# Kernel tuning notes

Measured on AMD Instinct MI355X. Metric: run time of the kernel, lower is better.

Reference implementation:

```python
import jax, jax.numpy as jnp
import numpy as np

N = 100000
IN_DIM, HID_DIM, EMB_DIM = 128, 64, 32
E = 1600000


def _gcn_conv(x, W, b, src, tgt, n):
    """PyG GCNConv: linear transform, add self-loops, sym-normalized scatter-add.
    W: [in, out], b: [out]. src/tgt: [E'] incl. self-loops handled by caller."""
    h = x @ W  # [n, out] -- transform before propagate (PyG order)
    deg = jax.ops.segment_sum(jnp.ones_like(tgt, dtype=h.dtype), tgt, num_segments=n)
    dinv = jnp.where(deg > 0, jax.lax.rsqrt(deg), 0.0)
    norm = dinv[src] * dinv[tgt]  # [E']
    msgs = h[src] * norm[:, None]  # [E', out]
    out = jax.ops.segment_sum(msgs, tgt, num_segments=n)
    return out + b


def setup_inputs() -> dict:
    key = jax.random.key(0)
    ks = jax.random.split(key, 6)
    x = jax.random.normal(ks[0], (N, IN_DIM), dtype=jnp.float32)
    edge_index = jax.random.randint(ks[1], (2, E), 0, N, dtype=jnp.int64)
    s1 = 1.0 / np.sqrt(IN_DIM)
    s2 = 1.0 / np.sqrt(HID_DIM)
    W1 = jax.random.uniform(ks[2], (IN_DIM, HID_DIM), jnp.float32, -s1, s1)
    b1 = jnp.zeros((HID_DIM,), jnp.float32)
    W2 = jax.random.uniform(ks[3], (HID_DIM, EMB_DIM), jnp.float32, -s2, s2)
    b2 = jnp.zeros((EMB_DIM,), jnp.float32)
    return {"x": x, "W1": W1, "b1": b1, "W2": W2, "b2": b2, "edge_index": edge_index}


def reference(x, W1, b1, W2, b2, edge_index):
    n = x.shape[0]
    src, tgt = edge_index[0], edge_index[1]
    # add self-loops once (same graph used by both convs)
    loops = jnp.arange(n, dtype=edge_index.dtype)
    src_sl = jnp.concatenate([src, loops])
    tgt_sl = jnp.concatenate([tgt, loops])
    h = jax.nn.relu(_gcn_conv(x, W1, b1, src_sl, tgt_sl, n))
    z = _gcn_conv(h, W2, b2, src_sl, tgt_sl, n)  # [n, EMB_DIM]
    # decode on original edges: edge-wise dot product
    recon = jnp.sum(z[src] * z[tgt], axis=1)  # [E]
    return z, recon
```

## Files before the change

kernel.cpp:

```cpp
#include <hip/hip_runtime.h>
#include <hip/hip_fp16.h>
#include <math.h>


#define NBMAX 512
#define BSHIFT 8
#define BNODES 256
#define CH 4096
#define CAPSHIFT 13
#define CAP (1 << CAPSHIFT)

typedef _Float16 half8 __attribute__((ext_vector_type(8)));
typedef float floatx4 __attribute__((ext_vector_type(4)));

static inline int divup(int a, int b) { return (a + b - 1) / b; }

__device__ inline void acc8(__half2* a, float4 v) {
    const __half2* h = (const __half2*)&v;
    a[0] = __hadd2(a[0], h[0]);
    a[1] = __hadd2(a[1], h[1]);
    a[2] = __hadd2(a[2], h[2]);
    a[3] = __hadd2(a[3], h[3]);
}
__device__ inline unsigned short f2bf(float f) {
    unsigned u = __builtin_bit_cast(unsigned, f);
    u = (u + 0x7FFFu + ((u >> 16) & 1u)) >> 16;
    return (unsigned short)u;
}


__global__ void k_init(int* __restrict__ gcur, unsigned* __restrict__ hs_pad,
                       unsigned* __restrict__ zs_pad) {
    int t = threadIdx.x;
    for (int b = t; b < NBMAX; b += 256) gcur[b] = b << CAPSHIFT;
    if (t < 32) hs_pad[t] = 0;
    else if (t < 48) zs_pad[t - 32] = 0;
}


__global__ __launch_bounds__(256) void k_part(const int* __restrict__ src,
                                              const int* __restrict__ tgt,
                                              int* __restrict__ gcur,
                                              unsigned* __restrict__ ebuf, int E, int NB) {
    __shared__ int h[NBMAX];
    __shared__ int base[NBMAX];
    int tid = threadIdx.x;
    int e0 = blockIdx.x * CH;
    for (int b = tid; b < NB; b += 256) h[b] = 0;
    __syncthreads();
    unsigned pk[16];
    int sv[16];
#pragma unroll
    for (int r = 0; r < 4; r++) {
        int e = e0 + (r * 256 + tid) * 4;
        if (e + 3 < E) {
            int4 t4 = *(const int4*)(tgt + e);
            int4 s4 = *(const int4*)(src + e);
            int tv[4] = {t4.x, t4.y, t4.z, t4.w};
            int sw[4] = {s4.x, s4.y, s4.z, s4.w};
#pragma unroll
            for (int j = 0; j < 4; j++) {
                int t = tv[j];
                int b = t >> BSHIFT;
                int l = atomicAdd(&h[b], 1);
                pk[r * 4 + j] = ((unsigned)b << 21) |
                                ((unsigned)(t & (BNODES - 1)) << 12) | (unsigned)l;
                sv[r * 4 + j] = sw[j];
            }
        } else {
#pragma unroll
            for (int j = 0; j < 4; j++) {
                int ee = e + j;
                if (ee < E) {
                    int t = tgt[ee];
                    int b = t >> BSHIFT;
                    int l = atomicAdd(&h[b], 1);
                    pk[r * 4 + j] = ((unsigned)b << 21) |
                                    ((unsigned)(t & (BNODES - 1)) << 12) | (unsigned)l;
                    sv[r * 4 + j] = src[ee];
                } else {
                    pk[r * 4 + j] = 0xFFFFFFFFu;
                }
            }
        }
    }
    __syncthreads();
    for (int b = tid; b < NB; b += 256) {
        int c = h[b];
        base[b] = c ? atomicAdd(&gcur[b], c) : 0;
    }
    __syncthreads();
#pragma unroll
    for (int i = 0; i < 16; i++) {
        if (pk[i] != 0xFFFFFFFFu) {
            int b = pk[i] >> 21;
            unsigned lt = (pk[i] >> 12) & (BNODES - 1);
            int l = pk[i] & 4095;
            ebuf[base[b] + l] = (lt << 23) | (unsigned)sv[i];
        }
    }
}


__global__ __launch_bounds__(256) void k_bfill(const unsigned* __restrict__ ebuf,
                                               const int* __restrict__ gcur,
                                               int* __restrict__ rowbeg,
                                               int* __restrict__ rowend,
                                               int* __restrict__ col,
                                               float* __restrict__ dinv, int n) {
    __shared__ int s_cnt[BNODES];
    __shared__ int s_scan[BNODES];
    __shared__ int s_cur[BNODES];
    int b = blockIdx.x, tid = threadIdx.x;
    int nbase = b << BSHIFT;
    int ebase = b << CAPSHIFT;
    int eend = gcur[b];
    s_cnt[tid] = 0;
    __syncthreads();
    for (int e = ebase + tid; e < eend; e += BNODES) {
        atomicAdd(&s_cnt[ebuf[e] >> 23], 1);
    }
    __syncthreads();
    s_scan[tid] = s_cnt[tid];
    __syncthreads();
    for (int off = 1; off < BNODES; off <<= 1) {
        int t = (tid >= off) ? s_scan[tid - off] : 0;
        __syncthreads();
        s_scan[tid] += t;
        __syncthreads();
    }
    int excl = s_scan[tid] - s_cnt[tid];
    s_cur[tid] = excl;
    int node = nbase + tid;
    if (node < n) {
        rowbeg[node] = ebase + excl;
        rowend[node] = ebase + excl + s_cnt[tid];
        dinv[node] = rsqrtf((float)(s_cnt[tid] + 1));
    }
    __syncthreads();
    for (int e = ebase + tid; e < eend; e += BNODES) {
        unsigned p = ebuf[e];
        int pos = atomicAdd(&s_cur[p >> 23], 1);
        col[ebase + pos] = (int)(p & 0x7FFFFFu);
    }
}


__global__ __launch_bounds__(256) void k_mm1(const float* __restrict__ x,
                                             const float* __restrict__ W1,
                                             const float* __restrict__ dinv,
                                             __half* __restrict__ hs, int n) {
    __shared__ _Float16 xh[64 * 136];
    __shared__ _Float16 Wt[64 * 136];
    int tid = threadIdx.x;
    int nbase = blockIdx.x * 64;
#pragma unroll
    for (int i = 0; i < 8; i++) {
        int f = tid + i * 256;
        int r = f >> 5, c4 = f & 31;
        int node = nbase + r;
        float4 v = make_float4(0.f, 0.f, 0.f, 0.f);
        if (node < n) v = *(const float4*)(x + (size_t)node * 128 + c4 * 4);
        union { uint2 u; __half2 h[2]; } pk;
        pk.h[0] = __floats2half2_rn(v.x, v.y);
        pk.h[1] = __floats2half2_rn(v.z, v.w);
        *(uint2*)&xh[r * 136 + c4 * 4] = pk.u;
    }
#pragma unroll
    for (int i = 0; i < 16; i++) {
        int f = tid + i * 256;
        int c = f & 63, kp = f >> 6;
        float a = W1[(size_t)(2 * kp) * 64 + c];
        float b = W1[(size_t)(2 * kp + 1) * 64 + c];
        *(__half2*)&Wt[c * 136 + 2 * kp] = __floats2half2_rn(a, b);
    }
    __syncthreads();
    int w = tid >> 6, lane = tid & 63;
    int quad = lane >> 4, m = lane & 15;
    floatx4 acc[4] = {{0.f, 0.f, 0.f, 0.f}, {0.f, 0.f, 0.f, 0.f},
                      {0.f, 0.f, 0.f, 0.f}, {0.f, 0.f, 0.f, 0.f}};
#pragma unroll
    for (int kt = 0; kt < 4; kt++) {
        half8 a = *(const half8*)&xh[(w * 16 + m) * 136 + kt * 32 + quad * 8];
#pragma unroll
        for (int ct = 0; ct < 4; ct++) {
            half8 b = *(const half8*)&Wt[(ct * 16 + m) * 136 + kt * 32 + quad * 8];
            acc[ct] = __builtin_amdgcn_mfma_f32_16x16x32_f16(a, b, acc[ct], 0, 0, 0);
        }
    }
#pragma unroll
    for (int reg = 0; reg < 4; reg++) {
        int node = nbase + w * 16 + quad * 4 + reg;
        if (node < n) {
            float d = dinv[node];
#pragma unroll
            for (int ct = 0; ct < 4; ct++) {
                hs[(size_t)node * 64 + ct * 16 + m] = __float2half(acc[ct][reg] * d);
            }
        }
    }
}


__global__ __launch_bounds__(256) void k_conv1(const __half* __restrict__ hs,
                                               const int* __restrict__ rowbeg,
                                               const int* __restrict__ rowend,
                                               const int* __restrict__ col,
                                               const float* __restrict__ dinv,
                                               const float* __restrict__ b1,
                                               __half* __restrict__ h2, int n) {
    int gw = (blockIdx.x * 256 + threadIdx.x) >> 6;
    int lane = threadIdx.x & 63;
    int q = lane >> 4, ln = lane & 15;
    int w = gw * 4 + q;
    if (w >= n) return;
    int qb = q << 4;
    int el = ln >> 3, fl = ln & 7;
    int beg = rowbeg[w], end = rowend[w];
    int deg = end - beg;
    int m = min(16, deg);
    int m2 = min(16, deg - 16);
    int sl = (ln < m) ? col[beg + ln] : 0;
    int sl2 = (ln < m2) ? col[beg + 16 + ln] : 0;
    __half2 a2[4];
#pragma unroll
    for (int j = 0; j < 4; j++) a2[j] = __half2half2(__float2half(0.f));
    int rs = (el == 0) ? w : n;
    float4 S = *(const float4*)(hs + (size_t)rs * 64 + fl * 8);
    float4 L[4];
#pragma unroll
    for (int r = 0; r < 4; r++) {
        int idx = 2 * r + el;
        int s = __shfl(sl, qb + idx);
        int a = (idx < m) ? s : n;
        L[r] = *(const float4*)(hs + (size_t)a * 64 + fl * 8);
    }
    acc8(a2, S);
#pragma unroll
    for (int r = 0; r < 4; r++) acc8(a2, L[r]);
#pragma unroll
    for (int r = 0; r < 4; r++) {
        int idx = 8 + 2 * r + el;
        int s = __shfl(sl, qb + idx);
        int a = (idx < m) ? s : n;
        L[r] = *(const float4*)(hs + (size_t)a * 64 + fl * 8);
    }
#pragma unroll
    for (int r = 0; r < 4; r++) acc8(a2, L[r]);
    if (deg > 16) {
#pragma unroll
        for (int r = 0; r < 4; r++) {
            int idx = 2 * r + el;
            int s = __shfl(sl2, qb + idx);
            int a = (idx < m2) ? s : n;
            L[r] = *(const float4*)(hs + (size_t)a * 64 + fl * 8);
        }
#pragma unroll
        for (int r = 0; r < 4; r++) acc8(a2, L[r]);
#pragma unroll
        for (int r = 0; r < 4; r++) {
            int idx = 8 + 2 * r + el;
            int s = __shfl(sl2, qb + idx);
            int a = (idx < m2) ? s : n;
            L[r] = *(const float4*)(hs + (size_t)a * 64 + fl * 8);
        }
#pragma unroll
        for (int r = 0; r < 4; r++) acc8(a2, L[r]);
    }
    if (deg > 32) {
        for (int b0 = 32; b0 < deg; b0 += 16) {
            int mc = min(16, deg - b0);
            int sl3 = (ln < mc) ? col[beg + b0 + ln] : 0;
            for (int r = 0; r < 8; r++) {
                int idx = 2 * r + el;
                int s = __shfl(sl3, qb + idx);
                int a = (idx < mc) ? s : n;
                float4 v = *(const float4*)(hs + (size_t)a * 64 + fl * 8);
                acc8(a2, v);
            }
        }
    }
    float r[8];
#pragma unroll
    for (int j = 0; j < 4; j++) {
        float2 f = __half22float2(a2[j]);
        r[2 * j] = f.x;
        r[2 * j + 1] = f.y;
    }
#pragma unroll
    for (int j = 0; j < 8; j++) r[j] += __shfl_xor(r[j], 8);

    if (el == 0) {
        float d = dinv[w];
        float4 bb0 = *(const float4*)(b1 + fl * 8);
        float4 bb1 = *(const float4*)(b1 + fl * 8 + 4);
        union { float4 f; __half2 h[4]; } u;
        u.h[0] = __floats2half2_rn(fmaxf(r[0] * d + bb0.x, 0.f),
                                   fmaxf(r[1] * d + bb0.y, 0.f));
        u.h[1] = __floats2half2_rn(fmaxf(r[2] * d + bb0.z, 0.f),
                                   fmaxf(r[3] * d + bb0.w, 0.f));
        u.h[2] = __floats2half2_rn(fmaxf(r[4] * d + bb1.x, 0.f),
                                   fmaxf(r[5] * d + bb1.y, 0.f));
        u.h[3] = __floats2half2_rn(fmaxf(r[6] * d + bb1.z, 0.f),
                                   fmaxf(r[7] * d + bb1.w, 0.f));
        *(float4*)(h2 + (size_t)w * 64 + fl * 8) = u.f;
    }
}


__global__ __launch_bounds__(256) void k_mm2(const __half* __restrict__ h2,
                                             const float* __restrict__ W2,
                                             const float* __restrict__ dinv,
                                             __half* __restrict__ zs, int n) {
    __shared__ _Float16 Wt[32 * 72];
    int tid = threadIdx.x;
    int nbase = blockIdx.x * 64;
#pragma unroll
    for (int i = 0; i < 4; i++) {
        int f = tid + i * 256;
        int c = f & 31, kp = f >> 5;
        float a = W2[(size_t)(2 * kp) * 32 + c];
        float b = W2[(size_t)(2 * kp + 1) * 32 + c];
        *(__half2*)&Wt[c * 72 + 2 * kp] = __floats2half2_rn(a, b);
    }
    __syncthreads();
    int w = tid >> 6, lane = tid & 63;
    int quad = lane >> 4, m = lane & 15;
    int arow = nbase + w * 16 + m;
    const __half* abase = h2 + (size_t)min(arow, n - 1) * 64;
    floatx4 acc[2] = {{0.f, 0.f, 0.f, 0.f}, {0.f, 0.f, 0.f, 0.f}};
#pragma unroll
    for (int kt = 0; kt < 2; kt++) {
        half8 a = *(const half8*)(abase + kt * 32 + quad * 8);
#pragma unroll
        for (int ct = 0; ct < 2; ct++) {
            half8 b = *(const half8*)&Wt[(ct * 16 + m) * 72 + kt * 32 + quad * 8];
            acc[ct] = __builtin_amdgcn_mfma_f32_16x16x32_f16(a, b, acc[ct], 0, 0, 0);
        }
    }
#pragma unroll
    for (int reg = 0; reg < 4; reg++) {
        int node = nbase + w * 16 + quad * 4 + reg;
        if (node < n) {
            float d = dinv[node];
#pragma unroll
            for (int ct = 0; ct < 2; ct++) {
                zs[(size_t)node * 32 + ct * 16 + m] = __float2half(acc[ct][reg] * d);
            }
        }
    }
}


__global__ __launch_bounds__(256) void k_conv2(const __half* __restrict__ zs,
                                               const int* __restrict__ rowbeg,
                                               const int* __restrict__ rowend,
                                               const int* __restrict__ col,
                                               const float* __restrict__ dinv,
                                               const float* __restrict__ b2,
                                               float* __restrict__ zout,
                                               unsigned short* __restrict__ zh, int n) {
    int gw = (blockIdx.x * 256 + threadIdx.x) >> 6;
    int lane = threadIdx.x & 63;
    int q = lane >> 4, ln = lane & 15;
    int w = gw * 4 + q;
    if (w >= n) return;
    int qb = q << 4;
    int el = ln >> 2, fl = ln & 3;
    int beg = rowbeg[w], end = rowend[w];
    int deg = end - beg;
    int m = min(16, deg);
    int m2 = min(16, deg - 16);
    int sl = (ln < m) ? col[beg + ln] : 0;
    int sl2 = (ln < m2) ? col[beg + 16 + ln] : 0;
    __half2 a2[4];
#pragma unroll
    for (int j = 0; j < 4; j++) a2[j] = __half2half2(__float2half(0.f));
    int rs = (el == 0) ? w : n;
    float4 S = *(const float4*)(zs + (size_t)rs * 32 + fl * 8);
    float4 L[4];
#pragma unroll
    for (int r = 0; r < 4; r++) {
        int idx = 4 * r + el;
        int s = __shfl(sl, qb + idx);
        int a = (idx < m) ? s : n;
        L[r] = *(const float4*)(zs + (size_t)a * 32 + fl * 8);
    }
    acc8(a2, S);
#pragma unroll
    for (int r = 0; r < 4; r++) acc8(a2, L[r]);
    if (deg > 16) {
#pragma unroll
        for (int r = 0; r < 4; r++) {
            int idx = 4 * r + el;
            int s = __shfl(sl2, qb + idx);
            int a = (idx < m2) ? s : n;
            L[r] = *(const float4*)(zs + (size_t)a * 32 + fl * 8);
        }
#pragma unroll
        for (int r = 0; r < 4; r++) acc8(a2, L[r]);
    }
    if (deg > 32) {
        for (int b0 = 32; b0 < deg; b0 += 16) {
            int mc = min(16, deg - b0);
            int sl3 = (ln < mc) ? col[beg + b0 + ln] : 0;
            for (int r = 0; r < 4; r++) {
                int idx = 4 * r + el;
                int s = __shfl(sl3, qb + idx);
                int a = (idx < mc) ? s : n;
                float4 v = *(const float4*)(zs + (size_t)a * 32 + fl * 8);
                acc8(a2, v);
            }
        }
    }
    float r[8];
#pragma unroll
    for (int j = 0; j < 4; j++) {
        float2 f = __half22float2(a2[j]);
        r[2 * j] = f.x;
        r[2 * j + 1] = f.y;
    }
#pragma unroll
    for (int d = 4; d < 16; d <<= 1)
#pragma unroll
        for (int j = 0; j < 8; j++) r[j] += __shfl_xor(r[j], d);

    if (el == 0) {
        float d = dinv[w];
        float4 bb0 = *(const float4*)(b2 + fl * 8);
        float4 bb1 = *(const float4*)(b2 + fl * 8 + 4);
        float o0 = r[0] * d + bb0.x, o1 = r[1] * d + bb0.y;
        float o2 = r[2] * d + bb0.z, o3 = r[3] * d + bb0.w;
        float o4 = r[4] * d + bb1.x, o5 = r[5] * d + bb1.y;
        float o6 = r[6] * d + bb1.z, o7 = r[7] * d + bb1.w;
        *(float4*)(zout + (size_t)w * 32 + fl * 8) = make_float4(o0, o1, o2, o3);
        *(float4*)(zout + (size_t)w * 32 + fl * 8 + 4) = make_float4(o4, o5, o6, o7);
        uint4 p;
        p.x = (unsigned)f2bf(o0) | ((unsigned)f2bf(o1) << 16);
        p.y = (unsigned)f2bf(o2) | ((unsigned)f2bf(o3) << 16);
        p.z = (unsigned)f2bf(o4) | ((unsigned)f2bf(o5) << 16);
        p.w = (unsigned)f2bf(o6) | ((unsigned)f2bf(o7) << 16);
        *(uint4*)(zh + (size_t)w * 32 + fl * 8) = p;
    }
}


__device__ inline float bfdot8(uint4 a, uint4 b) {
    const unsigned* pa = (const unsigned*)&a;
    const unsigned* pb = (const unsigned*)&b;
    float v = 0.f;
#pragma unroll
    for (int w = 0; w < 4; w++) {
        float alo = __builtin_bit_cast(float, pa[w] << 16);
        float ahi = __builtin_bit_cast(float, pa[w] & 0xFFFF0000u);
        float blo = __builtin_bit_cast(float, pb[w] << 16);
        float bhi = __builtin_bit_cast(float, pb[w] & 0xFFFF0000u);
        v += alo * blo + ahi * bhi;
    }
    return v;
}

__global__ __launch_bounds__(256) void k_decode(const unsigned short* __restrict__ zh,
                                                const int* __restrict__ src,
                                                const int* __restrict__ tgt,
                                                float* __restrict__ recon, int E) {
    int g = (blockIdx.x * 256 + threadIdx.x) >> 2;
    int fl = threadIdx.x & 3;
    int e0 = g * 4;
    if (e0 >= E) return;
    int cnt = min(4, E - e0);
    int s[4], t[4];
#pragma unroll
    for (int q = 0; q < 4; q++) {
        int e = (q < cnt) ? e0 + q : e0;
        s[q] = src[e];
        t[q] = tgt[e];
    }
    uint4 Za[4], Zb[4];
#pragma unroll
    for (int q = 0; q < 4; q++) {
        Za[q] = *(const uint4*)(zh + (size_t)s[q] * 32 + fl * 8);
        Zb[q] = *(const uint4*)(zh + (size_t)t[q] * 32 + fl * 8);
    }
    float v[4];
#pragma unroll
    for (int q = 0; q < 4; q++) {
        float x = bfdot8(Za[q], Zb[q]);
        x += __shfl_xor(x, 1);
        x += __shfl_xor(x, 2);
        v[q] = x;
    }
    if (fl == 0) {
        if (cnt == 4) {
            *(float4*)(recon + e0) = make_float4(v[0], v[1], v[2], v[3]);
        } else {
            for (int q = 0; q < cnt; q++) recon[e0 + q] = v[q];
        }
    }
}

extern "C" void kernel_launch(void* const* d_in, const int* in_sizes, int n_in,
                              void* d_out, int out_size, void* d_ws, size_t ws_size,
                              hipStream_t stream) {
    const float* x = (const float*)d_in[0];
    const float* W1 = (const float*)d_in[1];
    const float* b1 = (const float*)d_in[2];
    const float* W2 = (const float*)d_in[3];
    const float* b2 = (const float*)d_in[4];
    const int* ei = (const int*)d_in[5];

    int N = in_sizes[0] / 128;
    int E = in_sizes[5] / 2;
    const int* src = ei;
    const int* tgt = ei + E;
    int NB = divup(N, BNODES);

    char* ws = (char*)d_ws;
    size_t off = 0;
    auto alloc = [&](size_t bytes) {
        size_t r = off;
        off += (bytes + 255) & ~(size_t)255;
        return r;
    };
    int* gcur = (int*)(ws + alloc(NBMAX * 4));
    unsigned* ebuf = (unsigned*)(ws + alloc((size_t)NB * CAP * 4));
    int* col = (int*)(ws + alloc((size_t)NB * CAP * 4));
    int* rowbeg = (int*)(ws + alloc((size_t)N * 4));
    int* rowend = (int*)(ws + alloc((size_t)N * 4));
    float* dinv = (float*)(ws + alloc((size_t)N * 4));
    __half* hs = (__half*)(ws + alloc((size_t)(N + 1) * 64 * 2));
    __half* h2 = (__half*)(ws + alloc((size_t)N * 64 * 2));
    __half* zs = (__half*)(ws + alloc((size_t)(N + 1) * 32 * 2));
    unsigned short* zh = (unsigned short*)(ws + alloc((size_t)N * 32 * 2));

    float* zout = (float*)d_out;
    float* recon = zout + (size_t)N * 32;

    k_init<<<1, 256, 0, stream>>>(gcur, (unsigned*)(hs + (size_t)N * 64),
                                  (unsigned*)(zs + (size_t)N * 32));
    k_part<<<divup(E, CH), 256, 0, stream>>>(src, tgt, gcur, ebuf, E, NB);
    k_bfill<<<NB, BNODES, 0, stream>>>(ebuf, gcur, rowbeg, rowend, col, dinv, N);

    k_mm1<<<divup(N, 64), 256, 0, stream>>>(x, W1, dinv, hs, N);
    k_conv1<<<divup(N, 16), 256, 0, stream>>>(hs, rowbeg, rowend, col, dinv, b1, h2, N);
    k_mm2<<<divup(N, 64), 256, 0, stream>>>(h2, W2, dinv, zs, N);
    k_conv2<<<divup(N, 16), 256, 0, stream>>>(zs, rowbeg, rowend, col, dinv, b2, zout, zh, N);
    k_decode<<<divup(E, 256), 256, 0, stream>>>(zh, src, tgt, recon, E);
}
```

Measured before the change: 228.0 us.

## Restructure edge partition into two-pass count-then-scatter with larger chunks

The partition kernel now does a counting pass over target indices, reserves global bucket ranges, then rereads the edges and scatters each one using a shared-memory atomic cursor. This replaces the single pass that kept 16 packed entries per thread in registers. Chunk size grows from 4096 to 16384 edges per block and the block grows to 512 threads, so there are fewer blocks and fewer global atomics on the bucket cursors. The cost is reading the target array twice, and edge order within a bucket is no longer deterministic.

```diff
diff --git a/kernel.cpp b/kernel.cpp
--- a/kernel.cpp
+++ b/kernel.cpp
@@ -6,7 +6,8 @@
 #define NBMAX 512
 #define BSHIFT 8
 #define BNODES 256
-#define CH 4096
+#define CH 16384
+#define PTH 512
 #define CAPSHIFT 13
 #define CAP (1 << CAPSHIFT)
 
@@ -38,7 +39,7 @@
 }
 
 
-__global__ __launch_bounds__(256) void k_part(const int* __restrict__ src,
+__global__ __launch_bounds__(PTH) void k_part(const int* __restrict__ src,
                                               const int* __restrict__ tgt,
                                               int* __restrict__ gcur,
                                               unsigned* __restrict__ ebuf, int E, int NB) {
@@ -46,13 +47,33 @@
     __shared__ int base[NBMAX];
     int tid = threadIdx.x;
     int e0 = blockIdx.x * CH;
-    for (int b = tid; b < NB; b += 256) h[b] = 0;
-    __syncthreads();
-    unsigned pk[16];
-    int sv[16];
-#pragma unroll
-    for (int r = 0; r < 4; r++) {
-        int e = e0 + (r * 256 + tid) * 4;
+    for (int b = tid; b < NB; b += PTH) h[b] = 0;
+    __syncthreads();
+#pragma unroll
+    for (int r = 0; r < 8; r++) {
+        int e = e0 + (r * PTH + tid) * 4;
+        if (e + 3 < E) {
+            int4 t4 = *(const int4*)(tgt + e);
+            atomicAdd(&h[t4.x >> BSHIFT], 1);
+            atomicAdd(&h[t4.y >> BSHIFT], 1);
+            atomicAdd(&h[t4.z >> BSHIFT], 1);
+            atomicAdd(&h[t4.w >> BSHIFT], 1);
+        } else {
+            for (int j = 0; j < 4; j++) {
+                int ee = e + j;
+                if (ee < E) atomicAdd(&h[tgt[ee] >> BSHIFT], 1);
+            }
+        }
+    }
+    __syncthreads();
+    for (int b = tid; b < NB; b += PTH) {
+        int c = h[b];
+        base[b] = c ? atomicAdd(&gcur[b], c) : 0;
+    }
+    __syncthreads();
+#pragma unroll
+    for (int r = 0; r < 8; r++) {
+        int e = e0 + (r * PTH + tid) * 4;
         if (e + 3 < E) {
             int4 t4 = *(const int4*)(tgt + e);
             int4 s4 = *(const int4*)(src + e);
@@ -61,42 +82,18 @@
 #pragma unroll
             for (int j = 0; j < 4; j++) {
                 int t = tv[j];
-                int b = t >> BSHIFT;
-                int l = atomicAdd(&h[b], 1);
-                pk[r * 4 + j] = ((unsigned)b << 21) |
-                                ((unsigned)(t & (BNODES - 1)) << 12) | (unsigned)l;
-                sv[r * 4 + j] = sw[j];
+                int pos = atomicAdd(&base[t >> BSHIFT], 1);
+                ebuf[pos] = ((unsigned)(t & (BNODES - 1)) << 23) | (unsigned)sw[j];
             }
         } else {
-#pragma unroll
             for (int j = 0; j < 4; j++) {
                 int ee = e + j;
                 if (ee < E) {
                     int t = tgt[ee];
-                    int b = t >> BSHIFT;
-                    int l = atomicAdd(&h[b], 1);
-                    pk[r * 4 + j] = ((unsigned)b << 21) |
-                                    ((unsigned)(t & (BNODES - 1)) << 12) | (unsigned)l;
-                    sv[r * 4 + j] = src[ee];
-                } else {
-                    pk[r * 4 + j] = 0xFFFFFFFFu;
+                    int pos = atomicAdd(&base[t >> BSHIFT], 1);
+                    ebuf[pos] = ((unsigned)(t & (BNODES - 1)) << 23) | (unsigned)src[ee];
                 }
             }
-        }
-    }
-    __syncthreads();
-    for (int b = tid; b < NB; b += 256) {
-        int c = h[b];
-        base[b] = c ? atomicAdd(&gcur[b], c) : 0;
-    }
-    __syncthreads();
-#pragma unroll
-    for (int i = 0; i < 16; i++) {
-        if (pk[i] != 0xFFFFFFFFu) {
-            int b = pk[i] >> 21;
-            unsigned lt = (pk[i] >> 12) & (BNODES - 1);
-            int l = pk[i] & 4095;
-            ebuf[base[b] + l] = (lt << 23) | (unsigned)sv[i];
         }
     }
 }
@@ -538,7 +535,7 @@
 
     k_init<<<1, 256, 0, stream>>>(gcur, (unsigned*)(hs + (size_t)N * 64),
                                   (unsigned*)(zs + (size_t)N * 32));
-    k_part<<<divup(E, CH), 256, 0, stream>>>(src, tgt, gcur, ebuf, E, NB);
+    k_part<<<divup(E, CH), PTH, 0, stream>>>(src, tgt, gcur, ebuf, E, NB);
     k_bfill<<<NB, BNODES, 0, stream>>>(ebuf, gcur, rowbeg, rowend, col, dinv, N);
 
     k_mm1<<<divup(N, 64), 256, 0, stream>>>(x, W1, dinv, hs, N);
```

New measurement: 227.4 us. About the same (-0.3%).
